# Optimization experiments

Hardware: AMD Instinct MI355X
Metric: run time of the kernel (lower is better)

Reference implementation:

```python
import jax, jax.numpy as jnp
import numpy as np

B, T, F, H = 4096, 60, 128, 256

def setup_inputs() -> dict:
    key = jax.random.key(0)
    ks = jax.random.split(key, 14)
    sk = 1.0 / np.sqrt(H)
    def unif(k, shape):
        return jax.random.uniform(k, shape, jnp.float32, -sk, sk)
    return {
        "x": jax.random.normal(ks[0], (B, T, F), jnp.float32),
        "Wf": unif(ks[1], (F + H, H)), "bf": unif(ks[2], (H,)),
        "Wu": unif(ks[3], (F + H, H)), "bu": unif(ks[4], (H,)),
        "Wc": unif(ks[5], (F + H, H)), "bc": unif(ks[6], (H,)),
        "Wo": unif(ks[7], (F + H, H)), "bo": unif(ks[8], (H,)),
        "Wd1": jax.random.normal(ks[9], (H, H), jnp.float32) * np.sqrt(2.0 / H),
        "bd1": jnp.zeros((H,), jnp.float32),
        "Wd2": jax.random.normal(ks[10], (H, 1), jnp.float32) * np.sqrt(2.0 / H),
        "bd2": jnp.zeros((1,), jnp.float32),
    }

def reference(x, Wf, bf, Wu, bu, Wc, bc, Wo, bo, Wd1, bd1, Wd2, bd2):
    b = x.shape[0]
    h0 = jnp.zeros((b, H), x.dtype)
    c0 = jnp.zeros((b, H), x.dtype)

    def step(carry, xt):
        h, c = carry
        z = jnp.concatenate([xt, h], axis=-1)  # [B, F+H]
        f = jax.nn.sigmoid(z @ Wf + bf)
        u = jax.nn.sigmoid(z @ Wu + bu)
        g = jnp.tanh(z @ Wc + bc)
        o = jax.nn.sigmoid(z @ Wo + bo)
        c_new = f * c + u * g
        h_new = o * jnp.tanh(c_new)
        return (h_new, c_new), None

    (h, _), _ = jax.lax.scan(step, (h0, c0), jnp.swapaxes(x, 0, 1))  # scan over T
    # dense head: two stacked linear layers, no intermediate activation
    out = (h @ Wd1 + bd1) @ Wd2 + bd2  # [B, 1]
    return out
```

## Files before the change

kernel.cpp:

```cpp
#include <hip/hip_runtime.h>


#define T_STEPS 60
#define F_DIM 128
#define H_DIM 256
#define B_DIM 4096
#define BC 16
#define ZQ 31.75f
#define L2E 1.44269504f

typedef __attribute__((ext_vector_type(4))) int intx4;

__device__ __forceinline__ int q8(float v) {
    return __float2int_rn(fminf(fmaxf(v, -127.f), 127.f));
}

__global__ __launch_bounds__(1024)
void prep_kernel(const float* __restrict__ Wf, const float* __restrict__ Wu,
                 const float* __restrict__ Wc, const float* __restrict__ Wo,
                 const float* __restrict__ Wd1, const float* __restrict__ bd1,
                 const float* __restrict__ Wd2, const float* __restrict__ bd2,
                 float* __restrict__ cscale, intx4* __restrict__ qpack,
                 float* __restrict__ vhead, float* __restrict__ shead,
                 const float* __restrict__ x, unsigned* __restrict__ qx) {
    const int t = threadIdx.x;
    const int b = blockIdx.x;
    if (b < 32) {
        __shared__ float red[64][32];
        __shared__ float fsc[32];
        const int g = b >> 3, ch = (b >> 2) & 1, qtr = b & 3;
        const float* W = (g == 0) ? Wf : (g == 1) ? Wu : (g == 2) ? Wc : Wo;
        const int c32 = t & 31;
        const int col = ch * 128 + qtr * 32 + c32;
        const int grp = t >> 5;
        float mx = 1e-20f, mh = 1e-20f;
#pragma unroll
        for (int i = 0; i < 4; ++i)
            mx = fmaxf(mx, fabsf(W[(size_t)(grp * 4 + i) * H_DIM + col]));
#pragma unroll
        for (int i = 0; i < 8; ++i)
            mh = fmaxf(mh, fabsf(W[(size_t)(128 + grp * 8 + i) * H_DIM + col]));
        red[grp][c32] = mx;
        red[32 + grp][c32] = mh;
        __syncthreads();
        if (t < 32) {
            float Mx = red[0][t], Mh = red[32][t];
#pragma unroll 8
            for (int i = 1; i < 32; ++i) {
                Mx = fmaxf(Mx, red[i][t]);
                Mh = fmaxf(Mh, red[32 + i][t]);
            }
            float cs = fmaxf(4.f * Mx, Mh) * (1.f / 16129.f);
            cscale[g * 256 + ch * 128 + qtr * 32 + t] = cs;
            fsc[t] = 1.f / (127.f * cs);
        }
        __syncthreads();
        if (t < 768) {
            int lane = t & 63, fr = t >> 6;
            int hli = fr / 6, ks6 = fr - hli * 6;
            int hl = qtr * 2 + hli;
            int l15 = lane & 15, quad = lane >> 4;
            int colw = ch * 128 + hl * 16 + l15;
            int k0 = ks6 * 64 + quad * 16;
            float f = ((ks6 < 2) ? 4.f : 1.f) * fsc[hli * 16 + l15];
            int w[4];
#pragma unroll
            for (int d = 0; d < 4; ++d) {
                int b0 = q8(W[(size_t)(k0 + d * 4 + 0) * H_DIM + colw] * f) & 255;
                int b1 = q8(W[(size_t)(k0 + d * 4 + 1) * H_DIM + colw] * f) & 255;
                int b2 = q8(W[(size_t)(k0 + d * 4 + 2) * H_DIM + colw] * f) & 255;
                int b3 = q8(W[(size_t)(k0 + d * 4 + 3) * H_DIM + colw] * f) & 255;
                w[d] = b0 | (b1 << 8) | (b2 << 16) | (b3 << 24);
            }
            intx4 v = {w[0], w[1], w[2], w[3]};
            qpack[(((ch * 8 + hl) * 4 + g) * 6 + ks6) * 64 + lane] = v;
        }
    } else if (b == 32) {
        __shared__ float hp[1024];
        const int j = t >> 2, q = t & 3;
        float s = 0.f;
        const float* row = Wd1 + (size_t)j * H_DIM + q * 64;
#pragma unroll
        for (int i = 0; i < 16; ++i) {
            float4 a = *(const float4*)(row + i * 4);
            float4 bb = *(const float4*)(Wd2 + q * 64 + i * 4);
            s += a.x * bb.x + a.y * bb.y + a.z * bb.z + a.w * bb.w;
        }
        hp[t] = s;
        __syncthreads();
        float vj = 0.f;
        if (q == 0) vj = hp[t] + hp[t + 1] + hp[t + 2] + hp[t + 3];
        __syncthreads();
        if (q == 0) vhead[j] = vj;
        if (t < 256) hp[t] = bd1[t] * Wd2[t];
        __syncthreads();
        for (int off = 128; off > 0; off >>= 1) {
            if (t < off) hp[t] += hp[t + off];
            __syncthreads();
        }
        if (t == 0) shead[0] = hp[0] + bd2[0];
    } else {
        const size_t NW = (size_t)B_DIM * T_STEPS * (F_DIM / 4);
        const size_t stride = (size_t)(gridDim.x - 33) * 1024;
        for (size_t w = (size_t)(b - 33) * 1024 + t; w < NW; w += stride) {
            float4 v = *(const float4*)(x + w * 4);
            unsigned u = (unsigned)(q8(v.x * ZQ) & 255) |
                         ((unsigned)(q8(v.y * ZQ) & 255) << 8) |
                         ((unsigned)(q8(v.z * ZQ) & 255) << 16) |
                         ((unsigned)(q8(v.w * ZQ) & 255) << 24);
            qx[w] = u;
        }
    }
}

template <bool USE_QX>
__global__ __launch_bounds__(512)
__attribute__((amdgpu_waves_per_eu(2, 2)))
void lstm_kernel(const float* __restrict__ x,
                 const float* __restrict__ bfv, const float* __restrict__ buv,
                 const float* __restrict__ bcv, const float* __restrict__ bov,
                 const intx4* __restrict__ qpack,
                 const float* __restrict__ cscale,
                 const float* __restrict__ vhead, const float* __restrict__ shead,
                 const unsigned* __restrict__ qx,
                 float* __restrict__ out)
{
    __shared__ __align__(16) intx4 wlds[64 * 64];
    __shared__ __align__(16) signed char zbuf[2][6][1024];
    __shared__ float rowsum[BC];

    const int tid  = threadIdx.x;
    const int wave = tid >> 6;
    const int lane = tid & 63;
    const int quad = lane >> 4;
    const int l15  = lane & 15;
    const int b0   = blockIdx.x * BC;

    for (int i = tid; i < 64 * 64; i += 512)
        wlds[i] = qpack[((i >> 6) * 6 + 5) * 64 + (i & 63)];
    intx4 wreg[5][8];
#pragma unroll
    for (int j = 0; j < 8; ++j)
#pragma unroll
        for (int ks = 0; ks < 5; ++ks) {
            intx4 v = qpack[(((8 * wave + j) * 6 + ks) * 64) + lane];
            int a0 = v[0], a1 = v[1], a2 = v[2], a3 = v[3];
            asm volatile("" : "+v"(a0), "+v"(a1), "+v"(a2), "+v"(a3));
            intx4 w = {a0, a1, a2, a3};
            wreg[ks][j] = w;
        }

    for (int i = tid; i < 2 * 6 * 1024 / 4; i += 512) ((int*)zbuf)[i] = 0;
    if (tid < BC) rowsum[tid] = 0.f;

    float csS[2][4], bS[2][4], vh[2];
    float creg[2][4] = {};
    int haddr[2];
#pragma unroll
    for (int hb = 0; hb < 2; ++hb) {
        int a = 2 * wave + hb;
        int hc = a * 16 + l15;
        vh[hb] = vhead[hc];
        haddr[hb] = (2 + (a >> 2)) * 1024 + (a & 3) * 256 + l15;
#pragma unroll
        for (int g = 0; g < 4; ++g) {
            float cs = cscale[g * 256 + hc];
            float bi = (g == 0 ? bfv : g == 1 ? buv : g == 2 ? bcv : bov)[hc];
            float m = (g == 2) ? (-2.f * L2E) : (-L2E);
            csS[hb][g] = m * cs;
            bS[hb][g] = m * bi;
        }
    }

    const int xm = tid >> 5, xi = tid & 31;
    const int f0 = xi * 4;
    const int xaddr = (f0 >> 6) * 1024 + ((f0 & 63) >> 4) * 256 + xm * 16 + (f0 & 15);
    const float* xp = x + (size_t)(b0 + xm) * T_STEPS * F_DIM + f0;
    const unsigned* qxp = qx + (size_t)(b0 + xm) * T_STEPS * (F_DIM / 4) + xi;

    __syncthreads();
    float4 xv;
    unsigned xu;
    if constexpr (USE_QX) {
        unsigned u0 = qxp[0];
        *(unsigned*)(&zbuf[0][0][0] + xaddr) = u0;
        xu = qxp[32];
    } else {
        xv = *(const float4*)(xp);
        unsigned u = (unsigned)(q8(xv.x * ZQ) & 255) | ((unsigned)(q8(xv.y * ZQ) & 255) << 8) |
                     ((unsigned)(q8(xv.z * ZQ) & 255) << 16) | ((unsigned)(q8(xv.w * ZQ) & 255) << 24);
        *(unsigned*)(&zbuf[0][0][0] + xaddr) = u;
        xv = *(const float4*)(xp + F_DIM);
    }
    __syncthreads();

#define GATE_CELL(hb, rr)                                                          \
    {                                                                              \
        float uf = fmaf((float)acc[(hb) * 4 + 0][rr], csS[hb][0], bS[hb][0]);      \
        float uu = fmaf((float)acc[(hb) * 4 + 1][rr], csS[hb][1], bS[hb][1]);      \
        float uc = fmaf((float)acc[(hb) * 4 + 2][rr], csS[hb][2], bS[hb][2]);      \
        float uo = fmaf((float)acc[(hb) * 4 + 3][rr], csS[hb][3], bS[hb][3]);      \
        float af = 1.f + __builtin_amdgcn_exp2f(uf);                               \
        float au = 1.f + __builtin_amdgcn_exp2f(uu);                               \
        float ac = 1.f + __builtin_amdgcn_exp2f(uc);                               \
        float ao = 1.f + __builtin_amdgcn_exp2f(uo);                               \
        float r1 = __builtin_amdgcn_rcpf(af * au);                                 \
        float r2 = __builtin_amdgcn_rcpf(ac * ao);                                 \
        float fg = au * r1;                                                        \
        float ug = af * r1;                                                        \
        float rc = ao * r2;                                                        \
        float og = ac * r2;                                                        \
        float cn = fmaf(fg, creg[hb][rr], fmaf(ug + ug, rc, -ug));                 \
        creg[hb][rr] = cn;                                                         \
        float rh = __builtin_amdgcn_rcpf(1.f + __builtin_amdgcn_exp2f(cn * (-2.f * L2E))); \
        float hn = fmaf(og + og, rh, -og);                                         \
        zw[haddr[hb] + (quad * 4 + (rr)) * 16] =                                   \
            (signed char)__float2int_rn(hn * 127.f);                               \
    }

    for (int t = 0; t < T_STEPS; ++t) {
        const int p = t & 1, pn = p ^ 1;
        const intx4* zr = (const intx4*)(&zbuf[p][0][0]);
        signed char* zw = &zbuf[pn][0][0];

        intx4 acc[8] = {};
#pragma unroll
        for (int ks = 0; ks < 5; ++ks) {
            intx4 a = zr[ks * 64 + lane];
#pragma unroll
            for (int j = 0; j < 8; ++j)
                acc[j] = __builtin_amdgcn_mfma_i32_16x16x64_i8(a, wreg[ks][j], acc[j], 0, 0, 0);
        }
        {
            intx4 a5 = zr[5 * 64 + lane];
#pragma unroll
            for (int j = 0; j < 8; ++j) {
                intx4 bw = wlds[(8 * wave + j) * 64 + lane];
                acc[j] = __builtin_amdgcn_mfma_i32_16x16x64_i8(a5, bw, acc[j], 0, 0, 0);
            }
        }

        if (t < T_STEPS - 1) {
            if constexpr (USE_QX) {
                *(unsigned*)(zw + xaddr) = xu;
                if (t < T_STEPS - 2)
                    xu = qxp[(size_t)(t + 2) * 32];
            } else {
                unsigned u = (unsigned)(q8(xv.x * ZQ) & 255) | ((unsigned)(q8(xv.y * ZQ) & 255) << 8) |
                             ((unsigned)(q8(xv.z * ZQ) & 255) << 16) | ((unsigned)(q8(xv.w * ZQ) & 255) << 24);
                *(unsigned*)(zw + xaddr) = u;
                if (t < T_STEPS - 2)
                    xv = *(const float4*)(xp + (size_t)(t + 2) * F_DIM);
            }

#pragma unroll
            for (int hb = 0; hb < 2; ++hb)
#pragma unroll
                for (int rr = 0; rr < 4; ++rr)
                    GATE_CELL(hb, rr);
        } else {
            float hs[4] = {0.f, 0.f, 0.f, 0.f};
#pragma unroll
            for (int hb = 0; hb < 2; ++hb)
#pragma unroll
                for (int rr = 0; rr < 4; ++rr) {
                    float uf = fmaf((float)acc[hb * 4 + 0][rr], csS[hb][0], bS[hb][0]);
                    float uu = fmaf((float)acc[hb * 4 + 1][rr], csS[hb][1], bS[hb][1]);
                    float uc = fmaf((float)acc[hb * 4 + 2][rr], csS[hb][2], bS[hb][2]);
                    float uo = fmaf((float)acc[hb * 4 + 3][rr], csS[hb][3], bS[hb][3]);
                    float af = 1.f + __builtin_amdgcn_exp2f(uf);
                    float au = 1.f + __builtin_amdgcn_exp2f(uu);
                    float ac = 1.f + __builtin_amdgcn_exp2f(uc);
                    float ao = 1.f + __builtin_amdgcn_exp2f(uo);
                    float r1 = __builtin_amdgcn_rcpf(af * au);
                    float r2 = __builtin_amdgcn_rcpf(ac * ao);
                    float fg = au * r1;
                    float ug = af * r1;
                    float rc = ao * r2;
                    float og = ac * r2;
                    float cn = fmaf(fg, creg[hb][rr], fmaf(ug + ug, rc, -ug));
                    float rh = __builtin_amdgcn_rcpf(1.f + __builtin_amdgcn_exp2f(cn * (-2.f * L2E)));
                    float hn = fmaf(og + og, rh, -og);
                    hs[rr] += hn * vh[hb];
                }
#pragma unroll
            for (int rr = 0; rr < 4; ++rr) {
                float s = hs[rr];
#pragma unroll
                for (int m = 1; m < 16; m <<= 1)
                    s += __shfl_xor(s, m, 64);
                if (l15 == 0)
                    atomicAdd(&rowsum[quad * 4 + rr], s);
            }
        }
        __syncthreads();
    }
#undef GATE_CELL

    if (tid < BC)
        out[b0 + tid] = rowsum[tid] + shead[0];
}

extern "C" void kernel_launch(void* const* d_in, const int* in_sizes, int n_in,
                              void* d_out, int out_size, void* d_ws, size_t ws_size,
                              hipStream_t stream) {
    (void)in_sizes; (void)n_in; (void)out_size;
    const float* x   = (const float*)d_in[0];
    const float* Wf  = (const float*)d_in[1];
    const float* bfv = (const float*)d_in[2];
    const float* Wu  = (const float*)d_in[3];
    const float* buv = (const float*)d_in[4];
    const float* Wc  = (const float*)d_in[5];
    const float* bcv = (const float*)d_in[6];
    const float* Wo  = (const float*)d_in[7];
    const float* bov = (const float*)d_in[8];
    const float* Wd1 = (const float*)d_in[9];
    const float* bd1 = (const float*)d_in[10];
    const float* Wd2 = (const float*)d_in[11];
    const float* bd2 = (const float*)d_in[12];

    char* ws = (char*)d_ws;
    intx4* qpack = (intx4*)ws;
    size_t off = (size_t)384 * 64 * 16;
    float* cscale = (float*)(ws + off); off += 1024 * 4;
    float* vhead  = (float*)(ws + off); off += 256 * 4;
    float* shead  = (float*)(ws + off); off += 16;
    unsigned* qx  = (unsigned*)(ws + off);
    const size_t qx_bytes = (size_t)B_DIM * T_STEPS * (F_DIM / 4) * 4;
    const bool use_qx = ws_size >= off + qx_bytes;

    prep_kernel<<<use_qx ? 545 : 33, 1024, 0, stream>>>(
        Wf, Wu, Wc, Wo, Wd1, bd1, Wd2, bd2, cscale, qpack, vhead, shead, x, qx);
    if (use_qx)
        lstm_kernel<true><<<256, 512, 0, stream>>>(x, bfv, buv, bcv, bov, qpack,
                                                   cscale, vhead, shead, qx,
                                                   (float*)d_out);
    else
        lstm_kernel<false><<<256, 512, 0, stream>>>(x, bfv, buv, bcv, bov, qpack,
                                                    cscale, vhead, shead, qx,
                                                    (float*)d_out);
}
```

Before: 334.1 us.

## Overlap next-step input MFMAs with gate math and drop x pre-quantization pass

Moves the input-projection MFMAs for step t+1 (x-part, k-slices 0-1) off the recurrent critical path: they are issued right after the gate nonlinearities of step t, with waves alternating the half order so matrix work interleaves with transcendental math. Each step then only runs the four h-dependent k-slices before the gates. The separate prep pass that pre-quantized all of x to int8 in workspace is removed, and x is quantized inline from float loads again. This saves one full read and write pass over x, but puts the quantization back inside the recurrent loop and adds an extra barrier per step.

```diff
diff --git a/kernel.cpp b/kernel.cpp
--- a/kernel.cpp
+++ b/kernel.cpp
@@ -4,7 +4,6 @@
 #define T_STEPS 60
 #define F_DIM 128
 #define H_DIM 256
-#define B_DIM 4096
 #define BC 16
 #define ZQ 31.75f
 #define L2E 1.44269504f
@@ -21,8 +20,7 @@
                  const float* __restrict__ Wd1, const float* __restrict__ bd1,
                  const float* __restrict__ Wd2, const float* __restrict__ bd2,
                  float* __restrict__ cscale, intx4* __restrict__ qpack,
-                 float* __restrict__ vhead, float* __restrict__ shead,
-                 const float* __restrict__ x, unsigned* __restrict__ qx) {
+                 float* __restrict__ vhead, float* __restrict__ shead) {
     const int t = threadIdx.x;
     const int b = blockIdx.x;
     if (b < 32) {
@@ -75,7 +73,7 @@
             intx4 v = {w[0], w[1], w[2], w[3]};
             qpack[(((ch * 8 + hl) * 4 + g) * 6 + ks6) * 64 + lane] = v;
         }
-    } else if (b == 32) {
+    } else {
         __shared__ float hp[1024];
         const int j = t >> 2, q = t & 3;
         float s = 0.f;
@@ -99,21 +97,9 @@
             __syncthreads();
         }
         if (t == 0) shead[0] = hp[0] + bd2[0];
-    } else {
-        const size_t NW = (size_t)B_DIM * T_STEPS * (F_DIM / 4);
-        const size_t stride = (size_t)(gridDim.x - 33) * 1024;
-        for (size_t w = (size_t)(b - 33) * 1024 + t; w < NW; w += stride) {
-            float4 v = *(const float4*)(x + w * 4);
-            unsigned u = (unsigned)(q8(v.x * ZQ) & 255) |
-                         ((unsigned)(q8(v.y * ZQ) & 255) << 8) |
-                         ((unsigned)(q8(v.z * ZQ) & 255) << 16) |
-                         ((unsigned)(q8(v.w * ZQ) & 255) << 24);
-            qx[w] = u;
-        }
     }
 }
 
-template <bool USE_QX>
 __global__ __launch_bounds__(512)
 __attribute__((amdgpu_waves_per_eu(2, 2)))
 void lstm_kernel(const float* __restrict__ x,
@@ -122,7 +108,6 @@
                  const intx4* __restrict__ qpack,
                  const float* __restrict__ cscale,
                  const float* __restrict__ vhead, const float* __restrict__ shead,
-                 const unsigned* __restrict__ qx,
                  float* __restrict__ out)
 {
     __shared__ __align__(16) intx4 wlds[64 * 64];
@@ -176,23 +161,31 @@
     const int f0 = xi * 4;
     const int xaddr = (f0 >> 6) * 1024 + ((f0 & 63) >> 4) * 256 + xm * 16 + (f0 & 15);
     const float* xp = x + (size_t)(b0 + xm) * T_STEPS * F_DIM + f0;
-    const unsigned* qxp = qx + (size_t)(b0 + xm) * T_STEPS * (F_DIM / 4) + xi;
 
     __syncthreads();
-    float4 xv;
-    unsigned xu;
-    if constexpr (USE_QX) {
-        unsigned u0 = qxp[0];
-        *(unsigned*)(&zbuf[0][0][0] + xaddr) = u0;
-        xu = qxp[32];
-    } else {
-        xv = *(const float4*)(xp);
+    float4 xv = *(const float4*)(xp);
+    {
         unsigned u = (unsigned)(q8(xv.x * ZQ) & 255) | ((unsigned)(q8(xv.y * ZQ) & 255) << 8) |
                      ((unsigned)(q8(xv.z * ZQ) & 255) << 16) | ((unsigned)(q8(xv.w * ZQ) & 255) << 24);
         *(unsigned*)(&zbuf[0][0][0] + xaddr) = u;
-        xv = *(const float4*)(xp + F_DIM);
-    }
+    }
+    xv = *(const float4*)(xp + F_DIM);
     __syncthreads();
+
+    const intx4 z4 = {0, 0, 0, 0};
+
+    intx4 acc[8];
+    {
+        const intx4* zr0 = (const intx4*)(&zbuf[0][0][0]);
+        intx4 ax0 = zr0[lane];
+        intx4 ax1 = zr0[64 + lane];
+#pragma unroll
+        for (int j = 0; j < 8; ++j)
+            acc[j] = __builtin_amdgcn_mfma_i32_16x16x64_i8(
+                ax1, wreg[1][j],
+                __builtin_amdgcn_mfma_i32_16x16x64_i8(ax0, wreg[0][j], z4, 0, 0, 0),
+                0, 0, 0);
+    }
 
 #define GATE_CELL(hb, rr)                                                          \
     {                                                                              \
@@ -218,84 +211,120 @@
             (signed char)__float2int_rn(hn * 127.f);                               \
     }
 
-    for (int t = 0; t < T_STEPS; ++t) {
-        const int p = t & 1, pn = p ^ 1;
+#define GATES(hb) { GATE_CELL(hb, 0) GATE_CELL(hb, 1) GATE_CELL(hb, 2) GATE_CELL(hb, 3) }
+#define XMF(j0)                                                                    \
+    {                                                                              \
+        _Pragma("unroll")                                                          \
+        for (int j = (j0); j < (j0) + 4; ++j)                                      \
+            acc[j] = __builtin_amdgcn_mfma_i32_16x16x64_i8(                        \
+                ax1, wreg[1][j],                                                   \
+                __builtin_amdgcn_mfma_i32_16x16x64_i8(ax0, wreg[0][j], z4, 0, 0, 0), \
+                0, 0, 0);                                                          \
+    }
+
+#pragma unroll 1
+    for (int t = 0; t < T_STEPS - 1; ++t) {
+        const int p = t & 1;
         const intx4* zr = (const intx4*)(&zbuf[p][0][0]);
-        signed char* zw = &zbuf[pn][0][0];
-
-        intx4 acc[8] = {};
-#pragma unroll
-        for (int ks = 0; ks < 5; ++ks) {
-            intx4 a = zr[ks * 64 + lane];
-#pragma unroll
-            for (int j = 0; j < 8; ++j)
-                acc[j] = __builtin_amdgcn_mfma_i32_16x16x64_i8(a, wreg[ks][j], acc[j], 0, 0, 0);
-        }
+        signed char* zw = &zbuf[p ^ 1][0][0];
+
+        intx4 ah0 = zr[2 * 64 + lane];
+        intx4 ah1 = zr[3 * 64 + lane];
+        intx4 ah2 = zr[4 * 64 + lane];
+        intx4 ah3 = zr[5 * 64 + lane];
         {
-            intx4 a5 = zr[5 * 64 + lane];
-#pragma unroll
-            for (int j = 0; j < 8; ++j) {
-                intx4 bw = wlds[(8 * wave + j) * 64 + lane];
-                acc[j] = __builtin_amdgcn_mfma_i32_16x16x64_i8(a5, bw, acc[j], 0, 0, 0);
+            unsigned u = (unsigned)(q8(xv.x * ZQ) & 255) | ((unsigned)(q8(xv.y * ZQ) & 255) << 8) |
+                         ((unsigned)(q8(xv.z * ZQ) & 255) << 16) | ((unsigned)(q8(xv.w * ZQ) & 255) << 24);
+            *(unsigned*)(zw + xaddr) = u;
+            if (t < T_STEPS - 2)
+                xv = *(const float4*)(xp + (size_t)(t + 2) * F_DIM);
+        }
+#pragma unroll
+        for (int j = 0; j < 8; ++j)
+            acc[j] = __builtin_amdgcn_mfma_i32_16x16x64_i8(ah0, wreg[2][j], acc[j], 0, 0, 0);
+#pragma unroll
+        for (int j = 0; j < 8; ++j)
+            acc[j] = __builtin_amdgcn_mfma_i32_16x16x64_i8(ah1, wreg[3][j], acc[j], 0, 0, 0);
+#pragma unroll
+        for (int j = 0; j < 8; ++j)
+            acc[j] = __builtin_amdgcn_mfma_i32_16x16x64_i8(ah2, wreg[4][j], acc[j], 0, 0, 0);
+#pragma unroll
+        for (int j = 0; j < 8; ++j)
+            acc[j] = __builtin_amdgcn_mfma_i32_16x16x64_i8(
+                ah3, wlds[(8 * wave + j) * 64 + lane], acc[j], 0, 0, 0);
+
+        __syncthreads();
+
+        const intx4* zn = (const intx4*)zw;
+        intx4 ax0 = zn[lane];
+        intx4 ax1 = zn[64 + lane];
+        if ((wave & 1) == 0) {
+            GATES(0) XMF(0) GATES(1) XMF(4)
+        } else {
+            GATES(1) XMF(4) GATES(0) XMF(0)
+        }
+
+        __syncthreads();
+    }
+
+    {
+        const intx4* zr = (const intx4*)(&zbuf[(T_STEPS - 1) & 1][0][0]);
+        intx4 ah0 = zr[2 * 64 + lane];
+        intx4 ah1 = zr[3 * 64 + lane];
+        intx4 ah2 = zr[4 * 64 + lane];
+        intx4 ah3 = zr[5 * 64 + lane];
+#pragma unroll
+        for (int j = 0; j < 8; ++j)
+            acc[j] = __builtin_amdgcn_mfma_i32_16x16x64_i8(ah0, wreg[2][j], acc[j], 0, 0, 0);
+#pragma unroll
+        for (int j = 0; j < 8; ++j)
+            acc[j] = __builtin_amdgcn_mfma_i32_16x16x64_i8(ah1, wreg[3][j], acc[j], 0, 0, 0);
+#pragma unroll
+        for (int j = 0; j < 8; ++j)
+            acc[j] = __builtin_amdgcn_mfma_i32_16x16x64_i8(ah2, wreg[4][j], acc[j], 0, 0, 0);
+#pragma unroll
+        for (int j = 0; j < 8; ++j)
+            acc[j] = __builtin_amdgcn_mfma_i32_16x16x64_i8(
+                ah3, wlds[(8 * wave + j) * 64 + lane], acc[j], 0, 0, 0);
+
+        float hs[4] = {0.f, 0.f, 0.f, 0.f};
+#pragma unroll
+        for (int hb = 0; hb < 2; ++hb)
+#pragma unroll
+            for (int rr = 0; rr < 4; ++rr) {
+                float uf = fmaf((float)acc[hb * 4 + 0][rr], csS[hb][0], bS[hb][0]);
+                float uu = fmaf((float)acc[hb * 4 + 1][rr], csS[hb][1], bS[hb][1]);
+                float uc = fmaf((float)acc[hb * 4 + 2][rr], csS[hb][2], bS[hb][2]);
+                float uo = fmaf((float)acc[hb * 4 + 3][rr], csS[hb][3], bS[hb][3]);
+                float af = 1.f + __builtin_amdgcn_exp2f(uf);
+                float au = 1.f + __builtin_amdgcn_exp2f(uu);
+                float ac = 1.f + __builtin_amdgcn_exp2f(uc);
+                float ao = 1.f + __builtin_amdgcn_exp2f(uo);
+                float r1 = __builtin_amdgcn_rcpf(af * au);
+                float r2 = __builtin_amdgcn_rcpf(ac * ao);
+                float fg = au * r1;
+                float ug = af * r1;
+                float rc = ao * r2;
+                float og = ac * r2;
+                float cn = fmaf(fg, creg[hb][rr], fmaf(ug + ug, rc, -ug));
+                float rh = __builtin_amdgcn_rcpf(1.f + __builtin_amdgcn_exp2f(cn * (-2.f * L2E)));
+                float hn = fmaf(og + og, rh, -og);
+                hs[rr] += hn * vh[hb];
             }
-        }
-
-        if (t < T_STEPS - 1) {
-            if constexpr (USE_QX) {
-                *(unsigned*)(zw + xaddr) = xu;
-                if (t < T_STEPS - 2)
-                    xu = qxp[(size_t)(t + 2) * 32];
-            } else {
-                unsigned u = (unsigned)(q8(xv.x * ZQ) & 255) | ((unsigned)(q8(xv.y * ZQ) & 255) << 8) |
-                             ((unsigned)(q8(xv.z * ZQ) & 255) << 16) | ((unsigned)(q8(xv.w * ZQ) & 255) << 24);
-                *(unsigned*)(zw + xaddr) = u;
-                if (t < T_STEPS - 2)
-                    xv = *(const float4*)(xp + (size_t)(t + 2) * F_DIM);
-            }
-
-#pragma unroll
-            for (int hb = 0; hb < 2; ++hb)
-#pragma unroll
-                for (int rr = 0; rr < 4; ++rr)
-                    GATE_CELL(hb, rr);
-        } else {
-            float hs[4] = {0.f, 0.f, 0.f, 0.f};
-#pragma unroll
-            for (int hb = 0; hb < 2; ++hb)
-#pragma unroll
-                for (int rr = 0; rr < 4; ++rr) {
-                    float uf = fmaf((float)acc[hb * 4 + 0][rr], csS[hb][0], bS[hb][0]);
-                    float uu = fmaf((float)acc[hb * 4 + 1][rr], csS[hb][1], bS[hb][1]);
-                    float uc = fmaf((float)acc[hb * 4 + 2][rr], csS[hb][2], bS[hb][2]);
-                    float uo = fmaf((float)acc[hb * 4 + 3][rr], csS[hb][3], bS[hb][3]);
-                    float af = 1.f + __builtin_amdgcn_exp2f(uf);
-                    float au = 1.f + __builtin_amdgcn_exp2f(uu);
-                    float ac = 1.f + __builtin_amdgcn_exp2f(uc);
-                    float ao = 1.f + __builtin_amdgcn_exp2f(uo);
-                    float r1 = __builtin_amdgcn_rcpf(af * au);
-                    float r2 = __builtin_amdgcn_rcpf(ac * ao);
-                    float fg = au * r1;
-                    float ug = af * r1;
-                    float rc = ao * r2;
-                    float og = ac * r2;
-                    float cn = fmaf(fg, creg[hb][rr], fmaf(ug + ug, rc, -ug));
-                    float rh = __builtin_amdgcn_rcpf(1.f + __builtin_amdgcn_exp2f(cn * (-2.f * L2E)));
-                    float hn = fmaf(og + og, rh, -og);
-                    hs[rr] += hn * vh[hb];
-                }
-#pragma unroll
-            for (int rr = 0; rr < 4; ++rr) {
-                float s = hs[rr];
-#pragma unroll
-                for (int m = 1; m < 16; m <<= 1)
-                    s += __shfl_xor(s, m, 64);
-                if (l15 == 0)
-                    atomicAdd(&rowsum[quad * 4 + rr], s);
-            }
+#pragma unroll
+        for (int rr = 0; rr < 4; ++rr) {
+            float s = hs[rr];
+#pragma unroll
+            for (int m = 1; m < 16; m <<= 1)
+                s += __shfl_xor(s, m, 64);
+            if (l15 == 0)
+                atomicAdd(&rowsum[quad * 4 + rr], s);
         }
         __syncthreads();
     }
 #undef GATE_CELL
+#undef GATES
+#undef XMF
 
     if (tid < BC)
         out[b0 + tid] = rowsum[tid] + shead[0];
@@ -304,7 +333,7 @@
 extern "C" void kernel_launch(void* const* d_in, const int* in_sizes, int n_in,
                               void* d_out, int out_size, void* d_ws, size_t ws_size,
                               hipStream_t stream) {
-    (void)in_sizes; (void)n_in; (void)out_size;
+    (void)in_sizes; (void)n_in; (void)out_size; (void)ws_size;
     const float* x   = (const float*)d_in[0];
     const float* Wf  = (const float*)d_in[1];
     const float* bfv = (const float*)d_in[2];
@@ -325,18 +354,9 @@
     float* cscale = (float*)(ws + off); off += 1024 * 4;
     float* vhead  = (float*)(ws + off); off += 256 * 4;
     float* shead  = (float*)(ws + off); off += 16;
-    unsigned* qx  = (unsigned*)(ws + off);
-    const size_t qx_bytes = (size_t)B_DIM * T_STEPS * (F_DIM / 4) * 4;
-    const bool use_qx = ws_size >= off + qx_bytes;
-
-    prep_kernel<<<use_qx ? 545 : 33, 1024, 0, stream>>>(
-        Wf, Wu, Wc, Wo, Wd1, bd1, Wd2, bd2, cscale, qpack, vhead, shead, x, qx);
-    if (use_qx)
-        lstm_kernel<true><<<256, 512, 0, stream>>>(x, bfv, buv, bcv, bov, qpack,
-                                                   cscale, vhead, shead, qx,
-                                                   (float*)d_out);
-    else
-        lstm_kernel<false><<<256, 512, 0, stream>>>(x, bfv, buv, bcv, bov, qpack,
-                                                    cscale, vhead, shead, qx,
-                                                    (float*)d_out);
+
+    prep_kernel<<<33, 1024, 0, stream>>>(Wf, Wu, Wc, Wo, Wd1, bd1, Wd2, bd2,
+                                         cscale, qpack, vhead, shead);
+    lstm_kernel<<<256, 512, 0, stream>>>(x, bfv, buv, bcv, bov, qpack, cscale,
+                                         vhead, shead, (float*)d_out);
 }
```

Measured after the change: 376.9 us. 1.13x slower.
